# Kernel optimization log

Measured on AMD Instinct MI355X. Metric: run time of the kernel, lower is better.

## Reference

```python
import jax, jax.numpy as jnp
import numpy as np

N_NODES = 50000
N_EDGES = 800000
D = 64
NEG_SLOPE = 0.2


def setup_inputs() -> dict:
    key = jax.random.key(0)
    ks = jax.random.split(key, 16)
    inp = {
        "t": jnp.zeros((1,), jnp.float32),
        "x": jax.random.normal(ks[0], (N_NODES, D), jnp.float32),
        "edge_index": jax.random.randint(ks[1], (2, N_EDGES), 0, N_NODES, jnp.int64),
    }
    # 3 GATConv layers (64->64, 64->64, 64->64), heads=1
    s = 1.0 / np.sqrt(D)
    for li, k0 in zip((1, 2, 3), (2, 6, 10)):
        inp[f"W{li}"] = jax.random.normal(ks[k0], (D, D), jnp.float32) * s
        inp[f"a_src{li}"] = jax.random.normal(ks[k0 + 1], (D,), jnp.float32) * s
        inp[f"a_dst{li}"] = jax.random.normal(ks[k0 + 2], (D,), jnp.float32) * s
        inp[f"b{li}"] = jnp.zeros((D,), jnp.float32)
    return inp


def _gat_conv(x, src, dst, W, a_src, a_dst, b):
    # h = W x  (PyG: lin(x)), per-edge attention, segment softmax over dst
    n = x.shape[0]
    h = x @ W                                   # [N, D]
    score = jax.nn.leaky_relu(h[src] @ a_src + h[dst] @ a_dst, NEG_SLOPE)  # [E]
    smax = jax.ops.segment_max(score, dst, num_segments=n)                 # [N]
    ex = jnp.exp(score - smax[dst])                                        # [E]
    denom = jax.ops.segment_sum(ex, dst, num_segments=n)                   # [N]
    alpha = ex / denom[dst]                                                # [E]
    out = jax.ops.segment_sum(alpha[:, None] * h[src], dst, num_segments=n)
    return out + b


def reference(t, x, edge_index, W1, a_src1, a_dst1, b1, W2, a_src2, a_dst2, b2, W3, a_src3, a_dst3, b3):
    n = x.shape[0]
    # PyG GATConv default add_self_loops=True
    loops = jnp.arange(n, dtype=edge_index.dtype)
    src = jnp.concatenate([edge_index[0], loops])
    dst = jnp.concatenate([edge_index[1], loops])
    h = _gat_conv(x, src, dst, W1, a_src1, a_dst1, b1)
    h = jax.nn.relu(h)
    h = _gat_conv(h, src, dst, W2, a_src2, a_dst2, b2)
    h = jax.nn.relu(h)
    h = _gat_conv(h, src, dst, W3, a_src3, a_dst3, b3)
    return h
```

## Files before the change

kernel.cpp:

```cpp
#include <hip/hip_runtime.h>
#include <hip/hip_fp16.h>

#define NN 50000
#define NE 800000
#define D 64
#define GB ((NN + 63) / 64)
#define GH 391
#define NBUCK ((NN + 127) >> 7)
#define CHUNK 4096
#define EBLKS ((NE + CHUNK - 1) / CHUNK)
#define CAPB 4096
#define ARENA_BYTES (16384 + 17408 + 4352 + 4352)

__device__ __forceinline__ float lrelu(float s) { return (s > 0.0f) ? s : 0.2f * s; }


__device__ __forceinline__ void bin_body(int blk, const int* __restrict__ ei,
                                         int* __restrict__ gcur,
                                         unsigned* __restrict__ pairs, char* arena) {
  int* cnt_loc = (int*)arena;
  int* base_loc = cnt_loc + NBUCK;
  int t = threadIdx.x;
  int e0 = blk * CHUNK;
  int n = (NE - e0 < CHUNK) ? (NE - e0) : CHUNK;
  int nv = n >> 2;
  const int4* d4 = (const int4*)(ei + NE + e0);
  const int4* s4 = (const int4*)(ei + e0);
  for (int i = t; i < NBUCK; i += 256) cnt_loc[i] = 0;
  __syncthreads();
  for (int i = t; i < nv; i += 256) {
    int4 v = d4[i];
    atomicAdd(&cnt_loc[v.x >> 7], 1);
    atomicAdd(&cnt_loc[v.y >> 7], 1);
    atomicAdd(&cnt_loc[v.z >> 7], 1);
    atomicAdd(&cnt_loc[v.w >> 7], 1);
  }
  __syncthreads();
  for (int i = t; i < NBUCK; i += 256) {
    int c = cnt_loc[i];
    base_loc[i] = c ? (i * CAPB + atomicAdd(&gcur[i], c)) : 0;
    cnt_loc[i] = 0;
  }
  __syncthreads();
  for (int i = t; i < nv; i += 256) {
    int4 sv = s4[i];
    int4 dv = d4[i];
#pragma unroll
    for (int e = 0; e < 4; ++e) {
      int src = (&sv.x)[e];
      int dst = (&dv.x)[e];
      int b = dst >> 7;
      int off = atomicAdd(&cnt_loc[b], 1);
      unsigned pk = ((unsigned)src << 7) | (unsigned)(dst & 127);
      __builtin_nontemporal_store(pk, &pairs[base_loc[b] + off]);
    }
  }
}

__device__ __forceinline__ void sort_body(int b, const unsigned* __restrict__ pairs,
                                          const int* __restrict__ gcur,
                                          int* __restrict__ row_start,
                                          int* __restrict__ deg,
                                          int* __restrict__ sorted_src, char* arena) {
  int* cnt = (int*)arena;
  int* exc = cnt + 128;
  int* cur = exc + 128;
  int* buf = cur + 128;
  int t = threadIdx.x;
  int n0 = b << 7;
  int start = b * CAPB;
  int cntb = gcur[b];
  if (cntb > CAPB) cntb = CAPB;
  int nv = cntb >> 2;
  const uint4* p4 = (const uint4*)(pairs + start);
  if (t < 128) cnt[t] = 0;
  __syncthreads();
  for (int i = t; i < nv; i += 256) {
    uint4 v = p4[i];
    atomicAdd(&cnt[v.x & 127u], 1);
    atomicAdd(&cnt[v.y & 127u], 1);
    atomicAdd(&cnt[v.z & 127u], 1);
    atomicAdd(&cnt[v.w & 127u], 1);
  }
  for (int i = (nv << 2) + t; i < cntb; i += 256)
    atomicAdd(&cnt[pairs[start + i] & 127u], 1);
  __syncthreads();
  if (t < 128) exc[t] = cnt[t];
  __syncthreads();
  for (int s = 1; s < 128; s <<= 1) {
    int add = 0;
    if (t < 128 && t >= s) add = exc[t - s];
    __syncthreads();
    if (t < 128) exc[t] += add;
    __syncthreads();
  }
  if (t < 128) {
    int e = exc[t] - cnt[t];
    cur[t] = e;
    int nd = n0 + t;
    if (nd < NN) {
      row_start[nd] = start + e;
      deg[nd] = cnt[t];
    }
  }
  __syncthreads();
  for (int i = t; i < nv; i += 256) {
    uint4 v = p4[i];
#pragma unroll
    for (int e = 0; e < 4; ++e) {
      unsigned pk = (&v.x)[e];
      int pos = atomicAdd(&cur[pk & 127u], 1);
      if (pos < CAPB) buf[pos] = (int)(pk >> 7);
    }
  }
  for (int i = (nv << 2) + t; i < cntb; i += 256) {
    unsigned pk = pairs[start + i];
    int pos = atomicAdd(&cur[pk & 127u], 1);
    if (pos < CAPB) buf[pos] = (int)(pk >> 7);
  }
  __syncthreads();
  int4* o4 = (int4*)(sorted_src + start);
  const int4* b4 = (const int4*)buf;
  for (int i = t; i < nv; i += 256) o4[i] = b4[i];
  for (int i = (nv << 2) + t; i < cntb; i += 256)
    sorted_src[start + i] = buf[i];
}

__device__ __forceinline__ void gemm_body(int gblk, const float* __restrict__ xin,
                                          const float* __restrict__ W,
                                          const float* __restrict__ a_src,
                                          const float* __restrict__ a_dst,
                                          __half* __restrict__ h16,
                                          float* __restrict__ s_src,
                                          float* __restrict__ s_dst, int do_relu,
                                          char* arena) {
  float* wlds = (float*)arena;
  float (*xT)[68] = (float (*)[68])(arena + 16384);
  float (*psrc)[17] = (float (*)[17])(arena + 16384 + 17408);
  float (*pdst)[17] = (float (*)[17])(arena + 16384 + 17408 + 4352);
  int t = threadIdx.x;
  int n0 = gblk * 64;

  const float4* W4 = (const float4*)W;
  float4* wl4 = (float4*)wlds;
#pragma unroll
  for (int i = 0; i < 4; ++i) wl4[t + 256 * i] = W4[t + 256 * i];

#pragma unroll
  for (int i = 0; i < 4; ++i) {
    int idx = t + 256 * i;
    int r = idx >> 4, c4 = idx & 15;
    int n = n0 + r;
    float4 v = make_float4(0.f, 0.f, 0.f, 0.f);
    if (n < NN) v = ((const float4*)xin)[(size_t)n * 16 + c4];
    if (do_relu) {
      v.x = fmaxf(v.x, 0.f); v.y = fmaxf(v.y, 0.f);
      v.z = fmaxf(v.z, 0.f); v.w = fmaxf(v.w, 0.f);
    }
    xT[c4 * 4 + 0][r] = v.x;
    xT[c4 * 4 + 1][r] = v.y;
    xT[c4 * 4 + 2][r] = v.z;
    xT[c4 * 4 + 3][r] = v.w;
  }
  __syncthreads();

  int tr = t & 15, tc = t >> 4;
  float acc[4][4] = {};
#pragma unroll 8
  for (int k = 0; k < 64; ++k) {
    float4 xa = *(const float4*)&xT[k][tr * 4];
    float4 wv = *(const float4*)&wlds[k * 64 + tc * 4];
    float xs[4] = {xa.x, xa.y, xa.z, xa.w};
    float wj[4] = {wv.x, wv.y, wv.z, wv.w};
#pragma unroll
    for (int i = 0; i < 4; ++i)
#pragma unroll
      for (int j = 0; j < 4; ++j) acc[i][j] = fmaf(xs[i], wj[j], acc[i][j]);
  }

#pragma unroll
  for (int i = 0; i < 4; ++i) {
    int n = n0 + tr * 4 + i;
    if (n < NN) {
      __half2* dst = (__half2*)&h16[(size_t)n * 64 + tc * 4];
      dst[0] = __floats2half2_rn(acc[i][0], acc[i][1]);
      dst[1] = __floats2half2_rn(acc[i][2], acc[i][3]);
    }
  }

  float as[4], ad[4];
#pragma unroll
  for (int j = 0; j < 4; ++j) { as[j] = a_src[tc * 4 + j]; ad[j] = a_dst[tc * 4 + j]; }
#pragma unroll
  for (int i = 0; i < 4; ++i) {
    float p1 = 0.f, p2 = 0.f;
#pragma unroll
    for (int j = 0; j < 4; ++j) { p1 = fmaf(acc[i][j], as[j], p1); p2 = fmaf(acc[i][j], ad[j], p2); }
    psrc[tr * 4 + i][tc] = p1;
    pdst[tr * 4 + i][tc] = p2;
  }
  __syncthreads();
  if (t < 64) {
    int n = n0 + t;
    if (n < NN) {
      float s1 = 0.f, s2 = 0.f;
#pragma unroll
      for (int c = 0; c < 16; ++c) { s1 += psrc[t][c]; s2 += pdst[t][c]; }
      s_src[n] = s1;
      s_dst[n] = s2;
    }
  }
}


__global__ __launch_bounds__(256) void bin_gemm1(
    const int* __restrict__ ei, int* __restrict__ gcur, unsigned* __restrict__ pairs,
    const float* __restrict__ xin, const float* __restrict__ W,
    const float* __restrict__ a_src, const float* __restrict__ a_dst,
    __half* __restrict__ h16, float* __restrict__ s_src, float* __restrict__ s_dst) {
  __shared__ __align__(16) char arena[ARENA_BYTES];
  if (blockIdx.x < EBLKS) {
    bin_body(blockIdx.x, ei, gcur, pairs, arena);
  } else {
    gemm_body(blockIdx.x - EBLKS, xin, W, a_src, a_dst, h16, s_src, s_dst, 0, arena);
  }
}

__global__ __launch_bounds__(256) void sort_gemm1(
    const unsigned* __restrict__ pairs, const int* __restrict__ gcur,
    int* __restrict__ row_start, int* __restrict__ deg, int* __restrict__ sorted_src,
    const float* __restrict__ xin, const float* __restrict__ W,
    const float* __restrict__ a_src, const float* __restrict__ a_dst,
    __half* __restrict__ h16, float* __restrict__ s_src, float* __restrict__ s_dst) {
  __shared__ __align__(16) char arena[ARENA_BYTES];
  if (blockIdx.x < NBUCK) {
    sort_body(blockIdx.x, pairs, gcur, row_start, deg, sorted_src, arena);
  } else {
    gemm_body(blockIdx.x - NBUCK + GH, xin, W, a_src, a_dst, h16, s_src, s_dst, 0, arena);
  }
}

__global__ __launch_bounds__(256) void gemm_feat(
    const float* __restrict__ xin, const float* __restrict__ W,
    const float* __restrict__ a_src, const float* __restrict__ a_dst,
    __half* __restrict__ h16, float* __restrict__ s_src, float* __restrict__ s_dst,
    int do_relu) {
  __shared__ __align__(16) char arena[ARENA_BYTES];
  gemm_body(blockIdx.x, xin, W, a_src, a_dst, h16, s_src, s_dst, do_relu, arena);
}

__global__ void agg_kernel(const int* __restrict__ sorted_src, const int* __restrict__ row_start,
                           const int* __restrict__ deg, const float* __restrict__ s_src,
                           const float* __restrict__ s_dst, const __half* __restrict__ h16,
                           const float* __restrict__ bias, float* __restrict__ out) {
  int gid = blockIdx.x * blockDim.x + threadIdx.x;
  int n = gid >> 5;
  if (n >= NN) return;
  int lane = threadIdx.x & 31;
  int start = row_start[n];
  int dg = deg[n];
  float sdn = s_dst[n];
  float sself = lrelu(s_src[n] + sdn);
  float exself = __expf(sself - 8.0f);

  float2 acc;
  {
    float2 f = __half22float2(*(const __half2*)&h16[(size_t)n * 64 + 2 * lane]);
    acc.x = exself * f.x;
    acc.y = exself * f.y;
  }
  float dpart = 0.0f;
  for (int base = 0; base < dg; base += 32) {
    int i = base + lane;
    bool act = (i < dg);
    int msrc = act ? __builtin_nontemporal_load(&sorted_src[start + i]) : 0;
    float s = act ? lrelu(s_src[msrc] + sdn) : -INFINITY;
    float ex = __expf(s - 8.0f);
    dpart += ex;
    unsigned pk = ((unsigned)msrc << 16) |
                  (unsigned)__half_as_ushort(__float2half_rn(ex));
    int nch = (dg - base < 32) ? (dg - base) : 32;
    for (int b0 = 0; b0 < nch; b0 += 8) {
      unsigned pu[8]; unsigned vv[8];
#pragma unroll
      for (int e = 0; e < 8; ++e)
        pu[e] = __shfl(pk, b0 + e, 32);
#pragma unroll
      for (int e = 0; e < 8; ++e)
        vv[e] = *(const unsigned*)&h16[(size_t)(pu[e] >> 16) * 64 + 2 * lane];
#pragma unroll
      for (int e = 0; e < 8; ++e) {
        float xf = __half2float(__ushort_as_half((unsigned short)(pu[e] & 0xFFFFu)));
        float2 f = __half22float2(*(__half2*)&vv[e]);
        acc.x = fmaf(xf, f.x, acc.x);
        acc.y = fmaf(xf, f.y, acc.y);
      }
    }
  }
#pragma unroll
  for (int off = 16; off > 0; off >>= 1)
    dpart += __shfl_xor(dpart, off, 32);
  float d = exself + dpart;
  float2 bv = *(const float2*)&bias[2 * lane];
  float2 o;
  o.x = acc.x / d + bv.x;
  o.y = acc.y / d + bv.y;
  *(float2*)&out[(size_t)n * 64 + 2 * lane] = o;
}


extern "C" void kernel_launch(void* const* d_in, const int* in_sizes, int n_in,
                              void* d_out, int out_size, void* d_ws, size_t ws_size,
                              hipStream_t stream) {
  const float* x  = (const float*)d_in[1];
  const int*   ei = (const int*)d_in[2];
  const float* W1 = (const float*)d_in[3];
  const float* as1 = (const float*)d_in[4];
  const float* ad1 = (const float*)d_in[5];
  const float* b1 = (const float*)d_in[6];
  const float* W2 = (const float*)d_in[7];
  const float* as2 = (const float*)d_in[8];
  const float* ad2 = (const float*)d_in[9];
  const float* b2 = (const float*)d_in[10];
  const float* W3 = (const float*)d_in[11];
  const float* as3 = (const float*)d_in[12];
  const float* ad3 = (const float*)d_in[13];
  const float* b3 = (const float*)d_in[14];
  float* out = (float*)d_out;

  const size_t ND = (size_t)NN * D;
  char* base = (char*)d_ws;
  __half* h16    = (__half*)base;
  float* A       = (float*)(base + ND * 2);
  float* B       = A + ND;
  float* s_src   = B + ND;
  float* s_dst   = s_src + NN;
  int* row_start = (int*)(s_dst + NN);
  int* deg       = row_start + NN;
  int* gcur      = deg + NN;
  int* sorted_src= gcur + NBUCK;
  unsigned* pairs = (unsigned*)A;

  const int AGG_BLOCKS = (NN * 32 + 255) / 256;

  hipMemsetAsync(gcur, 0, (size_t)NBUCK * sizeof(int), stream);
  bin_gemm1<<<EBLKS + GH, 256, 0, stream>>>(ei, gcur, pairs, x, W1, as1, ad1,
                                            h16, s_src, s_dst);
  sort_gemm1<<<NBUCK + (GB - GH), 256, 0, stream>>>(pairs, gcur, row_start, deg, sorted_src,
                                                    x, W1, as1, ad1, h16, s_src, s_dst);

  agg_kernel<<<AGG_BLOCKS, 256, 0, stream>>>(sorted_src, row_start, deg, s_src, s_dst,
                                             h16, b1, A);
  gemm_feat<<<GB, 256, 0, stream>>>(A, W2, as2, ad2, h16, s_src, s_dst, 1);
  agg_kernel<<<AGG_BLOCKS, 256, 0, stream>>>(sorted_src, row_start, deg, s_src, s_dst,
                                             h16, b2, B);
  gemm_feat<<<GB, 256, 0, stream>>>(B, W3, as3, ad3, h16, s_src, s_dst, 1);
  agg_kernel<<<AGG_BLOCKS, 256, 0, stream>>>(sorted_src, row_start, deg, s_src, s_dst,
                                             h16, b3, out);
}
```

Measured before the change: 148.6 us.

## Fuse aggregation with next layer's GEMM into a single kernel

Merges each layer's edge aggregation (with bias and ReLU) with the following layer's feature transform and attention-score computation. Aggregated rows go straight into shared memory as the transposed GEMM input instead of being written to an fp32 buffer and read back. Ping-pong half-precision feature and score buffers avoid read/write hazards across blocks. This cuts two launches and the fp32 intermediate round trip, but the aggregation now runs 8 nodes per warp serially inside 782 blocks, so there is less parallelism for latency hiding.

```diff
diff --git a/kernel.cpp b/kernel.cpp
--- a/kernel.cpp
+++ b/kernel.cpp
@@ -126,44 +126,17 @@
     sorted_src[start + i] = buf[i];
 }
 
-__device__ __forceinline__ void gemm_body(int gblk, const float* __restrict__ xin,
-                                          const float* __restrict__ W,
-                                          const float* __restrict__ a_src,
+
+__device__ __forceinline__ void gemm_core(int n0, const float* __restrict__ a_src,
                                           const float* __restrict__ a_dst,
                                           __half* __restrict__ h16,
                                           float* __restrict__ s_src,
-                                          float* __restrict__ s_dst, int do_relu,
-                                          char* arena) {
+                                          float* __restrict__ s_dst, char* arena) {
   float* wlds = (float*)arena;
   float (*xT)[68] = (float (*)[68])(arena + 16384);
   float (*psrc)[17] = (float (*)[17])(arena + 16384 + 17408);
   float (*pdst)[17] = (float (*)[17])(arena + 16384 + 17408 + 4352);
   int t = threadIdx.x;
-  int n0 = gblk * 64;
-
-  const float4* W4 = (const float4*)W;
-  float4* wl4 = (float4*)wlds;
-#pragma unroll
-  for (int i = 0; i < 4; ++i) wl4[t + 256 * i] = W4[t + 256 * i];
-
-#pragma unroll
-  for (int i = 0; i < 4; ++i) {
-    int idx = t + 256 * i;
-    int r = idx >> 4, c4 = idx & 15;
-    int n = n0 + r;
-    float4 v = make_float4(0.f, 0.f, 0.f, 0.f);
-    if (n < NN) v = ((const float4*)xin)[(size_t)n * 16 + c4];
-    if (do_relu) {
-      v.x = fmaxf(v.x, 0.f); v.y = fmaxf(v.y, 0.f);
-      v.z = fmaxf(v.z, 0.f); v.w = fmaxf(v.w, 0.f);
-    }
-    xT[c4 * 4 + 0][r] = v.x;
-    xT[c4 * 4 + 1][r] = v.y;
-    xT[c4 * 4 + 2][r] = v.z;
-    xT[c4 * 4 + 3][r] = v.w;
-  }
-  __syncthreads();
-
   int tr = t & 15, tc = t >> 4;
   float acc[4][4] = {};
 #pragma unroll 8
@@ -177,7 +150,6 @@
 #pragma unroll
       for (int j = 0; j < 4; ++j) acc[i][j] = fmaf(xs[i], wj[j], acc[i][j]);
   }
-
 #pragma unroll
   for (int i = 0; i < 4; ++i) {
     int n = n0 + tr * 4 + i;
@@ -187,7 +159,6 @@
       dst[1] = __floats2half2_rn(acc[i][2], acc[i][3]);
     }
   }
-
   float as[4], ad[4];
 #pragma unroll
   for (int j = 0; j < 4; ++j) { as[j] = a_src[tc * 4 + j]; ad[j] = a_dst[tc * 4 + j]; }
@@ -210,6 +181,37 @@
       s_dst[n] = s2;
     }
   }
+}
+
+__device__ __forceinline__ void gemm_body(int gblk, const float* __restrict__ xin,
+                                          const float* __restrict__ W,
+                                          const float* __restrict__ a_src,
+                                          const float* __restrict__ a_dst,
+                                          __half* __restrict__ h16,
+                                          float* __restrict__ s_src,
+                                          float* __restrict__ s_dst, char* arena) {
+  float* wlds = (float*)arena;
+  float (*xT)[68] = (float (*)[68])(arena + 16384);
+  int t = threadIdx.x;
+  int n0 = gblk * 64;
+  const float4* W4 = (const float4*)W;
+  float4* wl4 = (float4*)wlds;
+#pragma unroll
+  for (int i = 0; i < 4; ++i) wl4[t + 256 * i] = W4[t + 256 * i];
+#pragma unroll
+  for (int i = 0; i < 4; ++i) {
+    int idx = t + 256 * i;
+    int r = idx >> 4, c4 = idx & 15;
+    int n = n0 + r;
+    float4 v = make_float4(0.f, 0.f, 0.f, 0.f);
+    if (n < NN) v = ((const float4*)xin)[(size_t)n * 16 + c4];
+    xT[c4 * 4 + 0][r] = v.x;
+    xT[c4 * 4 + 1][r] = v.y;
+    xT[c4 * 4 + 2][r] = v.z;
+    xT[c4 * 4 + 3][r] = v.w;
+  }
+  __syncthreads();
+  gemm_core(n0, a_src, a_dst, h16, s_src, s_dst, arena);
 }
 
 
@@ -222,7 +224,7 @@
   if (blockIdx.x < EBLKS) {
     bin_body(blockIdx.x, ei, gcur, pairs, arena);
   } else {
-    gemm_body(blockIdx.x - EBLKS, xin, W, a_src, a_dst, h16, s_src, s_dst, 0, arena);
+    gemm_body(blockIdx.x - EBLKS, xin, W, a_src, a_dst, h16, s_src, s_dst, arena);
   }
 }
 
@@ -236,17 +238,82 @@
   if (blockIdx.x < NBUCK) {
     sort_body(blockIdx.x, pairs, gcur, row_start, deg, sorted_src, arena);
   } else {
-    gemm_body(blockIdx.x - NBUCK + GH, xin, W, a_src, a_dst, h16, s_src, s_dst, 0, arena);
-  }
-}
-
-__global__ __launch_bounds__(256) void gemm_feat(
-    const float* __restrict__ xin, const float* __restrict__ W,
-    const float* __restrict__ a_src, const float* __restrict__ a_dst,
-    __half* __restrict__ h16, float* __restrict__ s_src, float* __restrict__ s_dst,
-    int do_relu) {
+    gemm_body(blockIdx.x - NBUCK + GH, xin, W, a_src, a_dst, h16, s_src, s_dst, arena);
+  }
+}
+
+__global__ __launch_bounds__(256) void agg_gemm(
+    const int* __restrict__ sorted_src, const int* __restrict__ row_start,
+    const int* __restrict__ deg, const float* __restrict__ ss_in,
+    const float* __restrict__ sd_in, const __half* __restrict__ h_in,
+    const float* __restrict__ bias,
+    const float* __restrict__ W, const float* __restrict__ a_src,
+    const float* __restrict__ a_dst, __half* __restrict__ h_out,
+    float* __restrict__ ss_out, float* __restrict__ sd_out) {
   __shared__ __align__(16) char arena[ARENA_BYTES];
-  gemm_body(blockIdx.x, xin, W, a_src, a_dst, h16, s_src, s_dst, do_relu, arena);
+  float* wlds = (float*)arena;
+  float (*xT)[68] = (float (*)[68])(arena + 16384);
+  int t = threadIdx.x;
+  int n0 = blockIdx.x * 64;
+  const float4* W4 = (const float4*)W;
+  float4* wl4 = (float4*)wlds;
+#pragma unroll
+  for (int i = 0; i < 4; ++i) wl4[t + 256 * i] = W4[t + 256 * i];
+
+  int g = t >> 5, lane = t & 31;
+  float2 bv = *(const float2*)&bias[2 * lane];
+  for (int i = 0; i < 8; ++i) {
+    int n = n0 + g * 8 + i;
+    float ox = 0.f, oy = 0.f;
+    if (n < NN) {
+      int start = row_start[n];
+      int dg = deg[n];
+      float sdn = sd_in[n];
+      float sself = lrelu(ss_in[n] + sdn);
+      float exself = __expf(sself - 8.0f);
+      float2 f0 = __half22float2(*(const __half2*)&h_in[(size_t)n * 64 + 2 * lane]);
+      float accx = exself * f0.x, accy = exself * f0.y;
+      float dpart = 0.0f;
+      for (int base = 0; base < dg; base += 32) {
+        int ii = base + lane;
+        bool act = (ii < dg);
+        int msrc = act ? __builtin_nontemporal_load(&sorted_src[start + ii]) : 0;
+        float s = act ? lrelu(ss_in[msrc] + sdn) : -INFINITY;
+        float ex = __expf(s - 8.0f);
+        dpart += ex;
+        unsigned pk = ((unsigned)msrc << 16) |
+                      (unsigned)__half_as_ushort(__float2half_rn(ex));
+        int nch = (dg - base < 32) ? (dg - base) : 32;
+        for (int b0 = 0; b0 < nch; b0 += 8) {
+          unsigned pu[8]; unsigned vv[8];
+#pragma unroll
+          for (int e = 0; e < 8; ++e)
+            pu[e] = __shfl(pk, b0 + e, 32);
+#pragma unroll
+          for (int e = 0; e < 8; ++e)
+            vv[e] = *(const unsigned*)&h_in[(size_t)(pu[e] >> 16) * 64 + 2 * lane];
+#pragma unroll
+          for (int e = 0; e < 8; ++e) {
+            float xf = __half2float(__ushort_as_half((unsigned short)(pu[e] & 0xFFFFu)));
+            float2 f = __half22float2(*(__half2*)&vv[e]);
+            accx = fmaf(xf, f.x, accx);
+            accy = fmaf(xf, f.y, accy);
+          }
+        }
+      }
+#pragma unroll
+      for (int off = 16; off > 0; off >>= 1)
+        dpart += __shfl_xor(dpart, off, 32);
+      float d = exself + dpart;
+      ox = fmaxf(accx / d + bv.x, 0.f);
+      oy = fmaxf(accy / d + bv.y, 0.f);
+    }
+    int nloc = g * 8 + i;
+    xT[2 * lane][nloc] = ox;
+    xT[2 * lane + 1][nloc] = oy;
+  }
+  __syncthreads();
+  gemm_core(n0, a_src, a_dst, h_out, ss_out, sd_out, arena);
 }
 
 __global__ void agg_kernel(const int* __restrict__ sorted_src, const int* __restrict__ row_start,
@@ -262,7 +329,6 @@
   float sdn = s_dst[n];
   float sself = lrelu(s_src[n] + sdn);
   float exself = __expf(sself - 8.0f);
-
   float2 acc;
   {
     float2 f = __half22float2(*(const __half2*)&h16[(size_t)n * 64 + 2 * lane]);
@@ -330,31 +396,31 @@
 
   const size_t ND = (size_t)NN * D;
   char* base = (char*)d_ws;
-  __half* h16    = (__half*)base;
-  float* A       = (float*)(base + ND * 2);
-  float* B       = A + ND;
-  float* s_src   = B + ND;
-  float* s_dst   = s_src + NN;
-  int* row_start = (int*)(s_dst + NN);
+  __half* h_a    = (__half*)base;
+  __half* h_b    = (__half*)(base + ND * 2);
+  float* ss_a    = (float*)(base + ND * 4);
+  float* sd_a    = ss_a + NN;
+  float* ss_b    = sd_a + NN;
+  float* sd_b    = ss_b + NN;
+  int* row_start = (int*)(sd_b + NN);
   int* deg       = row_start + NN;
   int* gcur      = deg + NN;
   int* sorted_src= gcur + NBUCK;
-  unsigned* pairs = (unsigned*)A;
+  unsigned* pairs = (unsigned*)h_b;
 
   const int AGG_BLOCKS = (NN * 32 + 255) / 256;
 
   hipMemsetAsync(gcur, 0, (size_t)NBUCK * sizeof(int), stream);
   bin_gemm1<<<EBLKS + GH, 256, 0, stream>>>(ei, gcur, pairs, x, W1, as1, ad1,
-                                            h16, s_src, s_dst);
+                                            h_a, ss_a, sd_a);
   sort_gemm1<<<NBUCK + (GB - GH), 256, 0, stream>>>(pairs, gcur, row_start, deg, sorted_src,
-                                                    x, W1, as1, ad1, h16, s_src, s_dst);
-
-  agg_kernel<<<AGG_BLOCKS, 256, 0, stream>>>(sorted_src, row_start, deg, s_src, s_dst,
-                                             h16, b1, A);
-  gemm_feat<<<GB, 256, 0, stream>>>(A, W2, as2, ad2, h16, s_src, s_dst, 1);
-  agg_kernel<<<AGG_BLOCKS, 256, 0, stream>>>(sorted_src, row_start, deg, s_src, s_dst,
-                                             h16, b2, B);
-  gemm_feat<<<GB, 256, 0, stream>>>(B, W3, as3, ad3, h16, s_src, s_dst, 1);
-  agg_kernel<<<AGG_BLOCKS, 256, 0, stream>>>(sorted_src, row_start, deg, s_src, s_dst,
-                                             h16, b3, out);
-}
+                                                    x, W1, as1, ad1, h_a, ss_a, sd_a);
+
+  agg_gemm<<<GB, 256, 0, stream>>>(sorted_src, row_start, deg, ss_a, sd_a, h_a, b1,
+                                   W2, as2, ad2, h_b, ss_b, sd_b);
+  agg_gemm<<<GB, 256, 0, stream>>>(sorted_src, row_start, deg, ss_b, sd_b, h_b, b2,
+                                   W3, as3, ad3, h_a, ss_a, sd_a);
+
+  agg_kernel<<<AGG_BLOCKS, 256, 0, stream>>>(sorted_src, row_start, deg, ss_a, sd_a,
+                                             h_a, b3, out);
+}
```

Measured after the change: 185.2 us. 24.6% more time.
